# Kernel tuning notes

Measured on AMD Instinct MI355X. Metric: run time of the kernel, lower is better.

Reference implementation:

```python
import jax, jax.numpy as jnp
import numpy as np

N = 100000
E = 1600000
IN, HID, OUT = 128, 128, 64


def sage_conv(x, edge_index, W_l, W_r, b):
    # PyG SAGEConv with mean aggregation:
    # out = mean_{j in N(i)} x_j @ W_l + x_i @ W_r + b
    src, dst = edge_index[0], edge_index[1]
    msgs = x[src]                                            # [E, D] gather
    summed = jax.ops.segment_sum(msgs, dst, num_segments=N)  # [N, D] scatter-add
    deg = jax.ops.segment_sum(jnp.ones((E,), x.dtype), dst, num_segments=N)
    mean = summed / jnp.maximum(deg, 1.0)[:, None]
    return mean @ W_l + x @ W_r + b


def setup_inputs() -> dict:
    key = jax.random.key(0)
    ks = jax.random.split(key, 8)
    x = jax.random.normal(ks[0], (N, IN), dtype=jnp.float32)
    edge_index = jax.random.randint(ks[1], (2, E), 0, N, dtype=jnp.int64)
    s1 = 1.0 / np.sqrt(IN)
    s2 = 1.0 / np.sqrt(HID)
    W1_l = jax.random.uniform(ks[2], (IN, HID), jnp.float32, -s1, s1)
    W1_r = jax.random.uniform(ks[3], (IN, HID), jnp.float32, -s1, s1)
    b1 = jnp.zeros((HID,), jnp.float32)
    W2_l = jax.random.uniform(ks[4], (HID, OUT), jnp.float32, -s2, s2)
    W2_r = jax.random.uniform(ks[5], (HID, OUT), jnp.float32, -s2, s2)
    b2 = jnp.zeros((OUT,), jnp.float32)
    return {"x": x, "edge_index": edge_index, "W1_l": W1_l, "W1_r": W1_r,
            "b1": b1, "W2_l": W2_l, "W2_r": W2_r, "b2": b2}


def reference(x, edge_index, W1_l, W1_r, b1, W2_l, W2_r, b2):
    h = sage_conv(x, edge_index, W1_l, W1_r, b1)
    h = jax.nn.relu(h)
    out = sage_conv(h, edge_index, W2_l, W2_r, b2)
    return out
```

## Files before the change

kernel.cpp:

```cpp
#include <hip/hip_runtime.h>

#define NN 100000
#define NE 1600000
#define KB 782
#define BSH 7
#define MAXB 4096
#define PBLK 400

#define OFF_CC    0
#define OFF_RST   1024
#define OFF_RDG   101120
#define OFF_STAGE 201216
#define OFF_XB    3404288
#define OFF_XF8   9810432
#define OFF_MEANB 13013504
#define OFF_W1LP  25825792
#define OFF_W1RP  (25825792 + 8192)
#define OFF_W2LP  (25825792 + 16384)
#define OFF_W2RP  (25825792 + 20480)

typedef __bf16 bf16x8 __attribute__((ext_vector_type(8)));
typedef float f32x4 __attribute__((ext_vector_type(4)));
typedef float f32x2 __attribute__((ext_vector_type(2)));

static __device__ __forceinline__ ushort f2bf(float f) {
    unsigned u = __float_as_uint(f);
    return (ushort)((u + 0x7fffu + ((u >> 16) & 1u)) >> 16);
}
static __device__ __forceinline__ float bflo(unsigned u) { return __uint_as_float(u << 16); }
static __device__ __forceinline__ float bfhi(unsigned u) { return __uint_as_float(u & 0xffff0000u); }

__global__ __launch_bounds__(1024) void cpart_kernel(const int* __restrict__ src,
                                                     const int* __restrict__ dst,
                                                     int* __restrict__ cc,
                                                     unsigned* __restrict__ stage) {
    __shared__ int hist[KB];
    __shared__ int cur[KB];
    int t = threadIdx.x;
    int e0 = blockIdx.x * (NE / PBLK);
    int e1 = e0 + (NE / PBLK);
    for (int i = t; i < KB; i += 1024) hist[i] = 0;
    __syncthreads();
    for (int e = e0 + t; e < e1; e += 1024)
        atomicAdd(&hist[dst[e] >> BSH], 1);
    __syncthreads();
    for (int i = t; i < KB; i += 1024) {
        int c = hist[i];
        cur[i] = c ? atomicAdd(&cc[i], c) : 0;
    }
    __syncthreads();
    for (int e = e0 + t; e < e1; e += 1024) {
        int d = dst[e];
        int bkt = d >> BSH;
        int p = atomicAdd(&cur[bkt], 1);
        if (p < MAXB)
            stage[bkt * MAXB + p] = ((unsigned)(d & 127) << 17) | (unsigned)src[e];
    }
}

#define F2_SORT  KB
#define F2_PACKB 6
#define F2_CVT   3125
#define F2_GRID  (F2_SORT + F2_PACKB + F2_CVT)

__global__ __launch_bounds__(1024) void fused2_kernel(
    unsigned* __restrict__ stage, const int* __restrict__ cc,
    int* __restrict__ rstart, int* __restrict__ rdeg,
    const float* __restrict__ x, ushort* __restrict__ xb, unsigned* __restrict__ xf8,
    const float* __restrict__ W1l, const float* __restrict__ W1r,
    const float* __restrict__ W2l, const float* __restrict__ W2r,
    ushort* __restrict__ w1lp, ushort* __restrict__ w1rp,
    ushort* __restrict__ w2lp, ushort* __restrict__ w2rp) {
    __shared__ unsigned ssrc[MAXB];
    __shared__ int sc[128];
    __shared__ int loff[129];
    __shared__ int lcur[128];
    int bid = blockIdx.x;
    int t = threadIdx.x;

    if (bid >= F2_SORT + F2_PACKB) {
        int i = (bid - F2_SORT - F2_PACKB) * 1024 + t;
        float4 v = ((const float4*)x)[i];
        uint2 o;
        o.x = (unsigned)f2bf(v.x) | ((unsigned)f2bf(v.y) << 16);
        o.y = (unsigned)f2bf(v.z) | ((unsigned)f2bf(v.w) << 16);
        ((uint2*)xb)[i] = o;
        int p8 = __builtin_amdgcn_cvt_pk_fp8_f32(v.x, v.y, 0, false);
        p8 = __builtin_amdgcn_cvt_pk_fp8_f32(v.z, v.w, p8, true);
        xf8[i] = (unsigned)p8;
        return;
    }

    if (bid >= F2_SORT) {
        int vb = (bid - F2_SORT) * 4 + (t >> 8);
        int vt = t & 255;
        const float* W;
        ushort* out;
        int N, frag0;
        if (vb < 8)       { W = W1l; out = w1lp; N = 128; frag0 = vb * 4; }
        else if (vb < 16) { W = W1r; out = w1rp; N = 128; frag0 = (vb - 8) * 4; }
        else if (vb < 20) { W = W2l; out = w2lp; N = 64;  frag0 = (vb - 16) * 4; }
        else              { W = W2r; out = w2rp; N = 64;  frag0 = (vb - 20) * 4; }
        int lane = vt & 63;
        int frag = frag0 + (vt >> 6);
        int NT = N >> 4;
        int ktile = frag / NT, ntile = frag - ktile * NT;
        int k = ktile * 32 + (lane >> 4) * 8;
        int n = ntile * 16 + (lane & 15);
        ushort tmp[8];
#pragma unroll
        for (int j = 0; j < 8; ++j) tmp[j] = f2bf(W[(k + j) * N + n]);
        uint4 o;
        o.x = (unsigned)tmp[0] | ((unsigned)tmp[1] << 16);
        o.y = (unsigned)tmp[2] | ((unsigned)tmp[3] << 16);
        o.z = (unsigned)tmp[4] | ((unsigned)tmp[5] << 16);
        o.w = (unsigned)tmp[6] | ((unsigned)tmp[7] << 16);
        *(uint4*)&out[(frag * 64 + lane) * 8] = o;
        return;
    }

    int b = bid;
    unsigned* st = stage + b * MAXB;
    int cnt = min(cc[b], MAXB);

    if (t < 128) lcur[t] = 0;
    __syncthreads();
    for (int i = t; i < cnt; i += 1024) atomicAdd(&lcur[st[i] >> 17], 1);
    __syncthreads();
    if (t < 128) sc[t] = lcur[t];
    __syncthreads();
    for (int off = 1; off < 128; off <<= 1) {
        int v = (t < 128 && t >= off) ? sc[t - off] : 0;
        __syncthreads();
        if (t < 128) sc[t] += v;
        __syncthreads();
    }
    if (t < 128) {
        int excl = (t == 0) ? 0 : sc[t - 1];
        loff[t] = excl;
        lcur[t] = excl;
    }
    if (t == 127) loff[128] = sc[127];
    __syncthreads();
    for (int i = t; i < cnt; i += 1024) {
        unsigned v = st[i];
        int p = atomicAdd(&lcur[v >> 17], 1);
        ssrc[p] = v & 0x1FFFFu;
    }
    __syncthreads();
    for (int i = t; i < cnt; i += 1024) st[i] = ssrc[i];
    int node0 = b << BSH;
    if (t < 128 && node0 + t < NN) {
        rstart[node0 + t] = b * MAXB + loff[t];
        rdeg[node0 + t] = loff[t + 1] - loff[t];
    }
}

static __device__ __forceinline__ void accum8(float* a, uint2 u) {
    f32x2 p0 = __builtin_amdgcn_cvt_pk_f32_fp8(u.x, false);
    f32x2 p1 = __builtin_amdgcn_cvt_pk_f32_fp8(u.x, true);
    f32x2 p2 = __builtin_amdgcn_cvt_pk_f32_fp8(u.y, false);
    f32x2 p3 = __builtin_amdgcn_cvt_pk_f32_fp8(u.y, true);
    a[0] += p0.x; a[1] += p0.y; a[2] += p1.x; a[3] += p1.y;
    a[4] += p2.x; a[5] += p2.y; a[6] += p3.x; a[7] += p3.y;
}

static __device__ __forceinline__ void writeRow8(ushort* __restrict__ meanb, int node,
                                                 int l4, const float* a, int deg) {
    float inv = 1.0f / fmaxf((float)deg, 1.0f);
    uint4 o;
    o.x = (unsigned)f2bf(a[0] * inv) | ((unsigned)f2bf(a[1] * inv) << 16);
    o.y = (unsigned)f2bf(a[2] * inv) | ((unsigned)f2bf(a[3] * inv) << 16);
    o.z = (unsigned)f2bf(a[4] * inv) | ((unsigned)f2bf(a[5] * inv) << 16);
    o.w = (unsigned)f2bf(a[6] * inv) | ((unsigned)f2bf(a[7] * inv) << 16);
    *(uint4*)&meanb[node * 128 + 8 * l4] = o;
}

__global__ __launch_bounds__(256) void agg1g_kernel(const unsigned* __restrict__ es,
                                                    const int* __restrict__ rstart,
                                                    const int* __restrict__ rdeg,
                                                    const unsigned* __restrict__ xf8,
                                                    ushort* __restrict__ meanb) {
    __shared__ unsigned eidx[MAXB];
    int t = threadIdx.x;
    int node0 = blockIdx.x * 32;
    int eBase = rstart[node0];
    int last = node0 + 31;
    int cnt = rstart[last] + rdeg[last] - eBase;
    for (int i = t; i < cnt; i += 256)
        eidx[i] = __builtin_nontemporal_load(&es[eBase + i]);
    __syncthreads();

    int l4 = t & 15;
    int nA = node0 + (t >> 4) * 2;
    int nB = nA + 1;
    int sA = rstart[nA] - eBase, dA = rdeg[nA];
    int sB = rstart[nB] - eBase, dB = rdeg[nB];
    const uint2* xv = (const uint2*)xf8;
    float aA[8] = {0.f, 0.f, 0.f, 0.f, 0.f, 0.f, 0.f, 0.f};
    float aB[8] = {0.f, 0.f, 0.f, 0.f, 0.f, 0.f, 0.f, 0.f};
    int eA = 0, eB = 0;
    while (eA + 4 <= dA && eB + 4 <= dB) {
        int qa0 = eidx[sA + eA + 0], qa1 = eidx[sA + eA + 1];
        int qa2 = eidx[sA + eA + 2], qa3 = eidx[sA + eA + 3];
        int qb0 = eidx[sB + eB + 0], qb1 = eidx[sB + eB + 1];
        int qb2 = eidx[sB + eB + 2], qb3 = eidx[sB + eB + 3];
        uint2 ua0 = xv[qa0 * 16 + l4], ua1 = xv[qa1 * 16 + l4];
        uint2 ua2 = xv[qa2 * 16 + l4], ua3 = xv[qa3 * 16 + l4];
        uint2 ub0 = xv[qb0 * 16 + l4], ub1 = xv[qb1 * 16 + l4];
        uint2 ub2 = xv[qb2 * 16 + l4], ub3 = xv[qb3 * 16 + l4];
        accum8(aA, ua0); accum8(aA, ua1); accum8(aA, ua2); accum8(aA, ua3);
        accum8(aB, ub0); accum8(aB, ub1); accum8(aB, ub2); accum8(aB, ub3);
        eA += 4; eB += 4;
    }
    for (; eA + 4 <= dA; eA += 4) {
        int q0 = eidx[sA + eA + 0], q1 = eidx[sA + eA + 1];
        int q2 = eidx[sA + eA + 2], q3 = eidx[sA + eA + 3];
        uint2 u0 = xv[q0 * 16 + l4], u1 = xv[q1 * 16 + l4];
        uint2 u2 = xv[q2 * 16 + l4], u3 = xv[q3 * 16 + l4];
        accum8(aA, u0); accum8(aA, u1); accum8(aA, u2); accum8(aA, u3);
    }
    for (; eA < dA; ++eA) accum8(aA, xv[eidx[sA + eA] * 16 + l4]);
    for (; eB + 4 <= dB; eB += 4) {
        int q0 = eidx[sB + eB + 0], q1 = eidx[sB + eB + 1];
        int q2 = eidx[sB + eB + 2], q3 = eidx[sB + eB + 3];
        uint2 u0 = xv[q0 * 16 + l4], u1 = xv[q1 * 16 + l4];
        uint2 u2 = xv[q2 * 16 + l4], u3 = xv[q3 * 16 + l4];
        accum8(aB, u0); accum8(aB, u1); accum8(aB, u2); accum8(aB, u3);
    }
    for (; eB < dB; ++eB) accum8(aB, xv[eidx[sB + eB] * 16 + l4]);

    writeRow8(meanb, nA, l4, aA, dA);
    writeRow8(meanb, nB, l4, aB, dB);
}

__global__ __launch_bounds__(256) void agg2g_kernel(const unsigned* __restrict__ es,
                                                    const int* __restrict__ rstart,
                                                    const int* __restrict__ rdeg,
                                                    const ushort* __restrict__ pb,
                                                    float* __restrict__ out) {
    __shared__ unsigned eidx[MAXB];
    int t = threadIdx.x;
    int node0 = blockIdx.x * 16;
    int eBase = rstart[node0];
    int last = node0 + 15;
    int cnt = rstart[last] + rdeg[last] - eBase;
    for (int i = t; i < cnt; i += 256)
        eidx[i] = __builtin_nontemporal_load(&es[eBase + i]);
    __syncthreads();

    int l5 = t & 31;
    int nA = node0 + (t >> 5) * 2;
    int nB = nA + 1;
    int sA = rstart[nA] - eBase, dA = rdeg[nA];
    int sB = rstart[nB] - eBase, dB = rdeg[nB];
    float2 pA = *(const float2*)&out[(size_t)nA * 64 + 2 * l5];
    float2 pB = *(const float2*)&out[(size_t)nB * 64 + 2 * l5];
    const unsigned* pbu = (const unsigned*)pb;
    float a0 = 0.f, a1 = 0.f, b0 = 0.f, b1 = 0.f;
    int eA = 0, eB = 0;
    while (eA + 4 <= dA && eB + 4 <= dB) {
        int qa0 = eidx[sA + eA + 0], qa1 = eidx[sA + eA + 1];
        int qa2 = eidx[sA + eA + 2], qa3 = eidx[sA + eA + 3];
        int qb0 = eidx[sB + eB + 0], qb1 = eidx[sB + eB + 1];
        int qb2 = eidx[sB + eB + 2], qb3 = eidx[sB + eB + 3];
        unsigned ua0 = pbu[qa0 * 32 + l5], ua1 = pbu[qa1 * 32 + l5];
        unsigned ua2 = pbu[qa2 * 32 + l5], ua3 = pbu[qa3 * 32 + l5];
        unsigned ub0 = pbu[qb0 * 32 + l5], ub1 = pbu[qb1 * 32 + l5];
        unsigned ub2 = pbu[qb2 * 32 + l5], ub3 = pbu[qb3 * 32 + l5];
        a0 += bflo(ua0) + bflo(ua1) + bflo(ua2) + bflo(ua3);
        a1 += bfhi(ua0) + bfhi(ua1) + bfhi(ua2) + bfhi(ua3);
        b0 += bflo(ub0) + bflo(ub1) + bflo(ub2) + bflo(ub3);
        b1 += bfhi(ub0) + bfhi(ub1) + bfhi(ub2) + bfhi(ub3);
        eA += 4; eB += 4;
    }
    for (; eA + 4 <= dA; eA += 4) {
        int q0 = eidx[sA + eA + 0], q1 = eidx[sA + eA + 1];
        int q2 = eidx[sA + eA + 2], q3 = eidx[sA + eA + 3];
        unsigned u0 = pbu[q0 * 32 + l5], u1 = pbu[q1 * 32 + l5];
        unsigned u2 = pbu[q2 * 32 + l5], u3 = pbu[q3 * 32 + l5];
        a0 += bflo(u0) + bflo(u1) + bflo(u2) + bflo(u3);
        a1 += bfhi(u0) + bfhi(u1) + bfhi(u2) + bfhi(u3);
    }
    for (; eA < dA; ++eA) {
        unsigned u = pbu[eidx[sA + eA] * 32 + l5];
        a0 += bflo(u); a1 += bfhi(u);
    }
    for (; eB + 4 <= dB; eB += 4) {
        int q0 = eidx[sB + eB + 0], q1 = eidx[sB + eB + 1];
        int q2 = eidx[sB + eB + 2], q3 = eidx[sB + eB + 3];
        unsigned u0 = pbu[q0 * 32 + l5], u1 = pbu[q1 * 32 + l5];
        unsigned u2 = pbu[q2 * 32 + l5], u3 = pbu[q3 * 32 + l5];
        b0 += bflo(u0) + bflo(u1) + bflo(u2) + bflo(u3);
        b1 += bfhi(u0) + bfhi(u1) + bfhi(u2) + bfhi(u3);
    }
    for (; eB < dB; ++eB) {
        unsigned u = pbu[eidx[sB + eB] * 32 + l5];
        b0 += bflo(u); b1 += bfhi(u);
    }
    float invA = 1.0f / fmaxf((float)dA, 1.0f);
    float invB = 1.0f / fmaxf((float)dB, 1.0f);
    float2 oA = {pA.x + a0 * invA, pA.y + a1 * invA};
    float2 oB = {pB.x + b0 * invB, pB.y + b1 * invB};
    *(float2*)&out[(size_t)nA * 64 + 2 * l5] = oA;
    *(float2*)&out[(size_t)nB * 64 + 2 * l5] = oB;
}

__global__ __launch_bounds__(256) void gemm1_kernel(const ushort* __restrict__ meanb,
                                                    const ushort* __restrict__ xb,
                                                    const ushort* __restrict__ w1lp,
                                                    const ushort* __restrict__ w1rp,
                                                    const float* __restrict__ b1,
                                                    const ushort* __restrict__ w2lp,
                                                    const ushort* __restrict__ w2rp,
                                                    const float* __restrict__ b2,
                                                    ushort* __restrict__ pb,
                                                    float* __restrict__ out) {
    __shared__ ushort As[64 * 136];
    __shared__ ushort Ws[16384];
    int t = threadIdx.x;
    int node0 = blockIdx.x * 64;
    int w = t >> 6, l = t & 63;
    int lrow = w * 16 + (l & 15);
    int lkq = (l >> 4) * 8;
    int cq = l & 15, rq = (l >> 4) * 4;

    f32x4 acc[8];
#pragma unroll
    for (int i = 0; i < 8; ++i) acc[i] = (f32x4){0.f, 0.f, 0.f, 0.f};

    {
        const uint4* g = (const uint4*)(meanb + (size_t)node0 * 128);
#pragma unroll
        for (int i = 0; i < 4; ++i) {
            int chunk = t + 256 * i;
            *(uint4*)&As[(chunk >> 4) * 136 + (chunk & 15) * 8] = g[chunk];
        }
        const uint4* wsrc = (const uint4*)w1lp;
#pragma unroll
        for (int i = 0; i < 8; ++i)
            ((uint4*)Ws)[t + 256 * i] = wsrc[t + 256 * i];
    }
    __syncthreads();
#pragma unroll
    for (int kt = 0; kt < 4; ++kt) {
        bf16x8 a = *(const bf16x8*)&As[lrow * 136 + kt * 32 + lkq];
        const bf16x8* bp = (const bf16x8*)Ws + (kt * 8) * 64 + l;
#pragma unroll
        for (int nt = 0; nt < 8; ++nt)
            acc[nt] = __builtin_amdgcn_mfma_f32_16x16x32_bf16(a, bp[nt * 64], acc[nt], 0, 0, 0);
    }
    __syncthreads();

    {
        const uint4* g = (const uint4*)(xb + (size_t)node0 * 128);
#pragma unroll
        for (int i = 0; i < 4; ++i) {
            int chunk = t + 256 * i;
            *(uint4*)&As[(chunk >> 4) * 136 + (chunk & 15) * 8] = g[chunk];
        }
        const uint4* wsrc = (const uint4*)w1rp;
#pragma unroll
        for (int i = 0; i < 8; ++i)
            ((uint4*)Ws)[t + 256 * i] = wsrc[t + 256 * i];
    }
    __syncthreads();
#pragma unroll
    for (int kt = 0; kt < 4; ++kt) {
        bf16x8 a = *(const bf16x8*)&As[lrow * 136 + kt * 32 + lkq];
        const bf16x8* bp = (const bf16x8*)Ws + (kt * 8) * 64 + l;
#pragma unroll
        for (int nt = 0; nt < 8; ++nt)
            acc[nt] = __builtin_amdgcn_mfma_f32_16x16x32_bf16(a, bp[nt * 64], acc[nt], 0, 0, 0);
    }
    __syncthreads();

#pragma unroll
    for (int nt = 0; nt < 8; ++nt) {
        int n = nt * 16 + cq;
        float bias = b1[n];
#pragma unroll
        for (int r = 0; r < 4; ++r) {
            float hv = fmaxf(acc[nt][r] + bias, 0.0f);
            As[(w * 16 + rq + r) * 136 + n] = f2bf(hv);
        }
    }
    {
        const uint4* wl = (const uint4*)w2lp;
        const uint4* wr = (const uint4*)w2rp;
#pragma unroll
        for (int i = 0; i < 4; ++i) {
            int chunk = t + 256 * i;
            ((uint4*)Ws)[chunk] = wl[chunk];
            ((uint4*)Ws)[1024 + chunk] = wr[chunk];
        }
    }
    __syncthreads();

    f32x4 acc2[4];
    f32x4 acc3[4];
#pragma unroll
    for (int i = 0; i < 4; ++i) {
        acc2[i] = (f32x4){0.f, 0.f, 0.f, 0.f};
        acc3[i] = (f32x4){0.f, 0.f, 0.f, 0.f};
    }
#pragma unroll
    for (int kt = 0; kt < 4; ++kt) {
        bf16x8 a = *(const bf16x8*)&As[lrow * 136 + kt * 32 + lkq];
        const bf16x8* bpl = (const bf16x8*)Ws + (kt * 4) * 64 + l;
        const bf16x8* bpr = (const bf16x8*)(Ws + 8192) + (kt * 4) * 64 + l;
#pragma unroll
        for (int nt = 0; nt < 4; ++nt) {
            acc2[nt] = __builtin_amdgcn_mfma_f32_16x16x32_bf16(a, bpl[nt * 64], acc2[nt], 0, 0, 0);
            acc3[nt] = __builtin_amdgcn_mfma_f32_16x16x32_bf16(a, bpr[nt * 64], acc3[nt], 0, 0, 0);
        }
    }

#pragma unroll
    for (int nt = 0; nt < 4; ++nt) {
        int n = nt * 16 + cq;
        float bias = b2[n];
#pragma unroll
        for (int r = 0; r < 4; ++r) {
            int row = node0 + w * 16 + rq + r;
            if (row < NN)
                out[(size_t)row * 64 + n] = acc3[nt][r] + bias;
        }
    }

    __syncthreads();
#pragma unroll
    for (int nt = 0; nt < 4; ++nt)
#pragma unroll
        for (int r = 0; r < 4; ++r)
            As[(w * 16 + rq + r) * 136 + nt * 16 + cq] = f2bf(acc2[nt][r]);
    __syncthreads();
    {
        uint4* g = (uint4*)(pb + (size_t)node0 * 64);
#pragma unroll
        for (int i = 0; i < 2; ++i) {
            int chunk = t + 256 * i;
            if (node0 + (chunk >> 3) < NN)
                g[chunk] = *(const uint4*)&As[(chunk >> 3) * 136 + (chunk & 7) * 8];
        }
    }
}

extern "C" void kernel_launch(void* const* d_in, const int* in_sizes, int n_in,
                              void* d_out, int out_size, void* d_ws, size_t ws_size,
                              hipStream_t stream) {
    const float* x   = (const float*)d_in[0];
    const int*   ei  = (const int*)d_in[1];
    const float* W1l = (const float*)d_in[2];
    const float* W1r = (const float*)d_in[3];
    const float* b1  = (const float*)d_in[4];
    const float* W2l = (const float*)d_in[5];
    const float* W2r = (const float*)d_in[6];
    const float* b2  = (const float*)d_in[7];

    const int* src = ei;
    const int* dst = ei + NE;

    int*      ws_i   = (int*)d_ws;
    int*      cc     = ws_i + OFF_CC;
    int*      rstart = ws_i + OFF_RST;
    int*      rdeg   = ws_i + OFF_RDG;
    unsigned* stage  = (unsigned*)(ws_i + OFF_STAGE);
    ushort*   xb     = (ushort*)(ws_i + OFF_XB);
    unsigned* xf8    = (unsigned*)(ws_i + OFF_XF8);
    ushort*   pb     = (ushort*)(ws_i + OFF_XF8);
    ushort*   meanb  = (ushort*)(ws_i + OFF_MEANB);
    ushort*   w1lp   = (ushort*)(ws_i + OFF_W1LP);
    ushort*   w1rp   = (ushort*)(ws_i + OFF_W1RP);
    ushort*   w2lp   = (ushort*)(ws_i + OFF_W2LP);
    ushort*   w2rp   = (ushort*)(ws_i + OFF_W2RP);

    (void)hipMemsetAsync(cc, 0, 1024 * sizeof(int), stream);

    cpart_kernel<<<PBLK, 1024, 0, stream>>>(src, dst, cc, stage);
    fused2_kernel<<<F2_GRID, 1024, 0, stream>>>(
        stage, cc, rstart, rdeg, x, xb, xf8,
        W1l, W1r, W2l, W2r, w1lp, w1rp, w2lp, w2rp);

    agg1g_kernel<<<NN / 32, 256, 0, stream>>>(stage, rstart, rdeg, xf8, meanb);
    gemm1_kernel<<<(NN + 63) / 64, 256, 0, stream>>>(meanb, xb, w1lp, w1rp, b1,
                                                     w2lp, w2rp, b2, pb, (float*)d_out);

    agg2g_kernel<<<NN / 16, 256, 0, stream>>>(stage, rstart, rdeg, pb, (float*)d_out);
}
```

Baseline: 236.6 us.

## Fuse layer-1 mean aggregation into the GEMM kernel via shared memory

Merges the layer-1 neighbor aggregation kernel with the dense GEMM kernel. Each 64-node block gathers its edge lists into the shared weight buffer, aggregates fp8 features directly into the shared A tile, then runs both layer-1 matmuls and the layer-2 projections. This removes one launch and the round trip of the bf16 mean matrix through global memory. In exchange, each block holds more shared memory and has less parallelism during the gather phase. The rstart/rdeg bounds guard is dropped so padded nodes get entries, and pb moves to a separate buffer.

```diff
diff --git a/kernel.cpp b/kernel.cpp
--- a/kernel.cpp
+++ b/kernel.cpp
@@ -150,11 +150,13 @@
     __syncthreads();
     for (int i = t; i < cnt; i += 1024) st[i] = ssrc[i];
     int node0 = b << BSH;
-    if (t < 128 && node0 + t < NN) {
+    if (t < 128) {
         rstart[node0 + t] = b * MAXB + loff[t];
         rdeg[node0 + t] = loff[t + 1] - loff[t];
     }
 }
+
+#define L1_GRID 1563
 
 static __device__ __forceinline__ void accum8(float* a, uint2 u) {
     f32x2 p0 = __builtin_amdgcn_cvt_pk_f32_fp8(u.x, false);
@@ -165,73 +167,182 @@
     a[4] += p2.x; a[5] += p2.y; a[6] += p3.x; a[7] += p3.y;
 }
 
-static __device__ __forceinline__ void writeRow8(ushort* __restrict__ meanb, int node,
-                                                 int l4, const float* a, int deg) {
-    float inv = 1.0f / fmaxf((float)deg, 1.0f);
-    uint4 o;
-    o.x = (unsigned)f2bf(a[0] * inv) | ((unsigned)f2bf(a[1] * inv) << 16);
-    o.y = (unsigned)f2bf(a[2] * inv) | ((unsigned)f2bf(a[3] * inv) << 16);
-    o.z = (unsigned)f2bf(a[4] * inv) | ((unsigned)f2bf(a[5] * inv) << 16);
-    o.w = (unsigned)f2bf(a[6] * inv) | ((unsigned)f2bf(a[7] * inv) << 16);
-    *(uint4*)&meanb[node * 128 + 8 * l4] = o;
-}
-
-__global__ __launch_bounds__(256) void agg1g_kernel(const unsigned* __restrict__ es,
-                                                    const int* __restrict__ rstart,
-                                                    const int* __restrict__ rdeg,
-                                                    const unsigned* __restrict__ xf8,
-                                                    ushort* __restrict__ meanb) {
-    __shared__ unsigned eidx[MAXB];
+__global__ __launch_bounds__(256) void l1_kernel(const unsigned* __restrict__ es,
+                                                 const int* __restrict__ rstart,
+                                                 const int* __restrict__ rdeg,
+                                                 const unsigned* __restrict__ xf8,
+                                                 const ushort* __restrict__ xb,
+                                                 const ushort* __restrict__ w1lp,
+                                                 const ushort* __restrict__ w1rp,
+                                                 const float* __restrict__ b1,
+                                                 const ushort* __restrict__ w2lp,
+                                                 const ushort* __restrict__ w2rp,
+                                                 const float* __restrict__ b2,
+                                                 ushort* __restrict__ pb,
+                                                 float* __restrict__ out) {
+    __shared__ ushort As[64 * 136];
+    __shared__ ushort WsBuf[16384];
+    unsigned* eidx = (unsigned*)WsBuf;
+
     int t = threadIdx.x;
-    int node0 = blockIdx.x * 32;
+    int node0 = blockIdx.x * 64;
+
     int eBase = rstart[node0];
-    int last = node0 + 31;
-    int cnt = rstart[last] + rdeg[last] - eBase;
+    int lastN = node0 + 63;
+    int cnt = rstart[lastN] + rdeg[lastN] - eBase;
     for (int i = t; i < cnt; i += 256)
         eidx[i] = __builtin_nontemporal_load(&es[eBase + i]);
     __syncthreads();
 
-    int l4 = t & 15;
-    int nA = node0 + (t >> 4) * 2;
-    int nB = nA + 1;
-    int sA = rstart[nA] - eBase, dA = rdeg[nA];
-    int sB = rstart[nB] - eBase, dB = rdeg[nB];
-    const uint2* xv = (const uint2*)xf8;
-    float aA[8] = {0.f, 0.f, 0.f, 0.f, 0.f, 0.f, 0.f, 0.f};
-    float aB[8] = {0.f, 0.f, 0.f, 0.f, 0.f, 0.f, 0.f, 0.f};
-    int eA = 0, eB = 0;
-    while (eA + 4 <= dA && eB + 4 <= dB) {
-        int qa0 = eidx[sA + eA + 0], qa1 = eidx[sA + eA + 1];
-        int qa2 = eidx[sA + eA + 2], qa3 = eidx[sA + eA + 3];
-        int qb0 = eidx[sB + eB + 0], qb1 = eidx[sB + eB + 1];
-        int qb2 = eidx[sB + eB + 2], qb3 = eidx[sB + eB + 3];
-        uint2 ua0 = xv[qa0 * 16 + l4], ua1 = xv[qa1 * 16 + l4];
-        uint2 ua2 = xv[qa2 * 16 + l4], ua3 = xv[qa3 * 16 + l4];
-        uint2 ub0 = xv[qb0 * 16 + l4], ub1 = xv[qb1 * 16 + l4];
-        uint2 ub2 = xv[qb2 * 16 + l4], ub3 = xv[qb3 * 16 + l4];
-        accum8(aA, ua0); accum8(aA, ua1); accum8(aA, ua2); accum8(aA, ua3);
-        accum8(aB, ub0); accum8(aB, ub1); accum8(aB, ub2); accum8(aB, ub3);
-        eA += 4; eB += 4;
-    }
-    for (; eA + 4 <= dA; eA += 4) {
-        int q0 = eidx[sA + eA + 0], q1 = eidx[sA + eA + 1];
-        int q2 = eidx[sA + eA + 2], q3 = eidx[sA + eA + 3];
-        uint2 u0 = xv[q0 * 16 + l4], u1 = xv[q1 * 16 + l4];
-        uint2 u2 = xv[q2 * 16 + l4], u3 = xv[q3 * 16 + l4];
-        accum8(aA, u0); accum8(aA, u1); accum8(aA, u2); accum8(aA, u3);
-    }
-    for (; eA < dA; ++eA) accum8(aA, xv[eidx[sA + eA] * 16 + l4]);
-    for (; eB + 4 <= dB; eB += 4) {
-        int q0 = eidx[sB + eB + 0], q1 = eidx[sB + eB + 1];
-        int q2 = eidx[sB + eB + 2], q3 = eidx[sB + eB + 3];
-        uint2 u0 = xv[q0 * 16 + l4], u1 = xv[q1 * 16 + l4];
-        uint2 u2 = xv[q2 * 16 + l4], u3 = xv[q3 * 16 + l4];
-        accum8(aB, u0); accum8(aB, u1); accum8(aB, u2); accum8(aB, u3);
-    }
-    for (; eB < dB; ++eB) accum8(aB, xv[eidx[sB + eB] * 16 + l4]);
-
-    writeRow8(meanb, nA, l4, aA, dA);
-    writeRow8(meanb, nB, l4, aB, dB);
+    {
+        int l4 = t & 15;
+        int g = t >> 4;
+        const uint2* xv = (const uint2*)xf8;
+#pragma unroll
+        for (int k = 0; k < 4; ++k) {
+            int nl = g * 4 + k;
+            int node = node0 + nl;
+            int s0 = rstart[node] - eBase;
+            int deg = rdeg[node];
+            float a[8] = {0.f, 0.f, 0.f, 0.f, 0.f, 0.f, 0.f, 0.f};
+            int e = 0;
+            for (; e + 4 <= deg; e += 4) {
+                int q0 = eidx[s0 + e + 0], q1 = eidx[s0 + e + 1];
+                int q2 = eidx[s0 + e + 2], q3 = eidx[s0 + e + 3];
+                uint2 u0 = xv[q0 * 16 + l4], u1 = xv[q1 * 16 + l4];
+                uint2 u2 = xv[q2 * 16 + l4], u3 = xv[q3 * 16 + l4];
+                accum8(a, u0); accum8(a, u1); accum8(a, u2); accum8(a, u3);
+            }
+            for (; e < deg; ++e) accum8(a, xv[eidx[s0 + e] * 16 + l4]);
+            float inv = 1.0f / fmaxf((float)deg, 1.0f);
+            uint4 o;
+            o.x = (unsigned)f2bf(a[0] * inv) | ((unsigned)f2bf(a[1] * inv) << 16);
+            o.y = (unsigned)f2bf(a[2] * inv) | ((unsigned)f2bf(a[3] * inv) << 16);
+            o.z = (unsigned)f2bf(a[4] * inv) | ((unsigned)f2bf(a[5] * inv) << 16);
+            o.w = (unsigned)f2bf(a[6] * inv) | ((unsigned)f2bf(a[7] * inv) << 16);
+            *(uint4*)&As[nl * 136 + 8 * l4] = o;
+        }
+    }
+    __syncthreads();
+
+    int w = t >> 6, l = t & 63;
+    int lrow = w * 16 + (l & 15);
+    int lkq = (l >> 4) * 8;
+    int cq = l & 15, rq = (l >> 4) * 4;
+
+    f32x4 acc[8];
+#pragma unroll
+    for (int i = 0; i < 8; ++i) acc[i] = (f32x4){0.f, 0.f, 0.f, 0.f};
+
+    {
+        const uint4* wsrc = (const uint4*)w1lp;
+#pragma unroll
+        for (int i = 0; i < 8; ++i)
+            ((uint4*)WsBuf)[t + 256 * i] = wsrc[t + 256 * i];
+    }
+    __syncthreads();
+#pragma unroll
+    for (int kt = 0; kt < 4; ++kt) {
+        bf16x8 a = *(const bf16x8*)&As[lrow * 136 + kt * 32 + lkq];
+        const bf16x8* bp = (const bf16x8*)WsBuf + (kt * 8) * 64 + l;
+#pragma unroll
+        for (int nt = 0; nt < 8; ++nt)
+            acc[nt] = __builtin_amdgcn_mfma_f32_16x16x32_bf16(a, bp[nt * 64], acc[nt], 0, 0, 0);
+    }
+    __syncthreads();
+
+    {
+        const uint4* g2 = (const uint4*)(xb + (size_t)node0 * 128);
+#pragma unroll
+        for (int i = 0; i < 4; ++i) {
+            int chunk = t + 256 * i;
+            *(uint4*)&As[(chunk >> 4) * 136 + (chunk & 15) * 8] = g2[chunk];
+        }
+        const uint4* wsrc = (const uint4*)w1rp;
+#pragma unroll
+        for (int i = 0; i < 8; ++i)
+            ((uint4*)WsBuf)[t + 256 * i] = wsrc[t + 256 * i];
+    }
+    __syncthreads();
+#pragma unroll
+    for (int kt = 0; kt < 4; ++kt) {
+        bf16x8 a = *(const bf16x8*)&As[lrow * 136 + kt * 32 + lkq];
+        const bf16x8* bp = (const bf16x8*)WsBuf + (kt * 8) * 64 + l;
+#pragma unroll
+        for (int nt = 0; nt < 8; ++nt)
+            acc[nt] = __builtin_amdgcn_mfma_f32_16x16x32_bf16(a, bp[nt * 64], acc[nt], 0, 0, 0);
+    }
+    __syncthreads();
+
+#pragma unroll
+    for (int nt = 0; nt < 8; ++nt) {
+        int n = nt * 16 + cq;
+        float bias = b1[n];
+#pragma unroll
+        for (int r = 0; r < 4; ++r) {
+            float hv = fmaxf(acc[nt][r] + bias, 0.0f);
+            As[(w * 16 + rq + r) * 136 + n] = f2bf(hv);
+        }
+    }
+    {
+        const uint4* wl = (const uint4*)w2lp;
+        const uint4* wr = (const uint4*)w2rp;
+#pragma unroll
+        for (int i = 0; i < 4; ++i) {
+            int chunk = t + 256 * i;
+            ((uint4*)WsBuf)[chunk] = wl[chunk];
+            ((uint4*)WsBuf)[1024 + chunk] = wr[chunk];
+        }
+    }
+    __syncthreads();
+
+    f32x4 acc2[4];
+    f32x4 acc3[4];
+#pragma unroll
+    for (int i = 0; i < 4; ++i) {
+        acc2[i] = (f32x4){0.f, 0.f, 0.f, 0.f};
+        acc3[i] = (f32x4){0.f, 0.f, 0.f, 0.f};
+    }
+#pragma unroll
+    for (int kt = 0; kt < 4; ++kt) {
+        bf16x8 a = *(const bf16x8*)&As[lrow * 136 + kt * 32 + lkq];
+        const bf16x8* bpl = (const bf16x8*)WsBuf + (kt * 4) * 64 + l;
+        const bf16x8* bpr = (const bf16x8*)(WsBuf + 8192) + (kt * 4) * 64 + l;
+#pragma unroll
+        for (int nt = 0; nt < 4; ++nt) {
+            acc2[nt] = __builtin_amdgcn_mfma_f32_16x16x32_bf16(a, bpl[nt * 64], acc2[nt], 0, 0, 0);
+            acc3[nt] = __builtin_amdgcn_mfma_f32_16x16x32_bf16(a, bpr[nt * 64], acc3[nt], 0, 0, 0);
+        }
+    }
+
+#pragma unroll
+    for (int nt = 0; nt < 4; ++nt) {
+        int n = nt * 16 + cq;
+        float bias = b2[n];
+#pragma unroll
+        for (int r = 0; r < 4; ++r) {
+            int row = node0 + w * 16 + rq + r;
+            if (row < NN)
+                out[(size_t)row * 64 + n] = acc3[nt][r] + bias;
+        }
+    }
+
+    __syncthreads();
+#pragma unroll
+    for (int nt = 0; nt < 4; ++nt)
+#pragma unroll
+        for (int r = 0; r < 4; ++r)
+            As[(w * 16 + rq + r) * 136 + nt * 16 + cq] = f2bf(acc2[nt][r]);
+    __syncthreads();
+    {
+        uint4* g2 = (uint4*)(pb + (size_t)node0 * 64);
+#pragma unroll
+        for (int i = 0; i < 2; ++i) {
+            int chunk = t + 256 * i;
+            if (node0 + (chunk >> 3) < NN)
+                g2[chunk] = *(const uint4*)&As[(chunk >> 3) * 136 + (chunk & 7) * 8];
+        }
+    }
 }
 
 __global__ __launch_bounds__(256) void agg2g_kernel(const unsigned* __restrict__ es,
@@ -306,146 +417,6 @@
     *(float2*)&out[(size_t)nB * 64 + 2 * l5] = oB;
 }
 
-__global__ __launch_bounds__(256) void gemm1_kernel(const ushort* __restrict__ meanb,
-                                                    const ushort* __restrict__ xb,
-                                                    const ushort* __restrict__ w1lp,
-                                                    const ushort* __restrict__ w1rp,
-                                                    const float* __restrict__ b1,
-                                                    const ushort* __restrict__ w2lp,
-                                                    const ushort* __restrict__ w2rp,
-                                                    const float* __restrict__ b2,
-                                                    ushort* __restrict__ pb,
-                                                    float* __restrict__ out) {
-    __shared__ ushort As[64 * 136];
-    __shared__ ushort Ws[16384];
-    int t = threadIdx.x;
-    int node0 = blockIdx.x * 64;
-    int w = t >> 6, l = t & 63;
-    int lrow = w * 16 + (l & 15);
-    int lkq = (l >> 4) * 8;
-    int cq = l & 15, rq = (l >> 4) * 4;
-
-    f32x4 acc[8];
-#pragma unroll
-    for (int i = 0; i < 8; ++i) acc[i] = (f32x4){0.f, 0.f, 0.f, 0.f};
-
-    {
-        const uint4* g = (const uint4*)(meanb + (size_t)node0 * 128);
-#pragma unroll
-        for (int i = 0; i < 4; ++i) {
-            int chunk = t + 256 * i;
-            *(uint4*)&As[(chunk >> 4) * 136 + (chunk & 15) * 8] = g[chunk];
-        }
-        const uint4* wsrc = (const uint4*)w1lp;
-#pragma unroll
-        for (int i = 0; i < 8; ++i)
-            ((uint4*)Ws)[t + 256 * i] = wsrc[t + 256 * i];
-    }
-    __syncthreads();
-#pragma unroll
-    for (int kt = 0; kt < 4; ++kt) {
-        bf16x8 a = *(const bf16x8*)&As[lrow * 136 + kt * 32 + lkq];
-        const bf16x8* bp = (const bf16x8*)Ws + (kt * 8) * 64 + l;
-#pragma unroll
-        for (int nt = 0; nt < 8; ++nt)
-            acc[nt] = __builtin_amdgcn_mfma_f32_16x16x32_bf16(a, bp[nt * 64], acc[nt], 0, 0, 0);
-    }
-    __syncthreads();
-
-    {
-        const uint4* g = (const uint4*)(xb + (size_t)node0 * 128);
-#pragma unroll
-        for (int i = 0; i < 4; ++i) {
-            int chunk = t + 256 * i;
-            *(uint4*)&As[(chunk >> 4) * 136 + (chunk & 15) * 8] = g[chunk];
-        }
-        const uint4* wsrc = (const uint4*)w1rp;
-#pragma unroll
-        for (int i = 0; i < 8; ++i)
-            ((uint4*)Ws)[t + 256 * i] = wsrc[t + 256 * i];
-    }
-    __syncthreads();
-#pragma unroll
-    for (int kt = 0; kt < 4; ++kt) {
-        bf16x8 a = *(const bf16x8*)&As[lrow * 136 + kt * 32 + lkq];
-        const bf16x8* bp = (const bf16x8*)Ws + (kt * 8) * 64 + l;
-#pragma unroll
-        for (int nt = 0; nt < 8; ++nt)
-            acc[nt] = __builtin_amdgcn_mfma_f32_16x16x32_bf16(a, bp[nt * 64], acc[nt], 0, 0, 0);
-    }
-    __syncthreads();
-
-#pragma unroll
-    for (int nt = 0; nt < 8; ++nt) {
-        int n = nt * 16 + cq;
-        float bias = b1[n];
-#pragma unroll
-        for (int r = 0; r < 4; ++r) {
-            float hv = fmaxf(acc[nt][r] + bias, 0.0f);
-            As[(w * 16 + rq + r) * 136 + n] = f2bf(hv);
-        }
-    }
-    {
-        const uint4* wl = (const uint4*)w2lp;
-        const uint4* wr = (const uint4*)w2rp;
-#pragma unroll
-        for (int i = 0; i < 4; ++i) {
-            int chunk = t + 256 * i;
-            ((uint4*)Ws)[chunk] = wl[chunk];
-            ((uint4*)Ws)[1024 + chunk] = wr[chunk];
-        }
-    }
-    __syncthreads();
-
-    f32x4 acc2[4];
-    f32x4 acc3[4];
-#pragma unroll
-    for (int i = 0; i < 4; ++i) {
-        acc2[i] = (f32x4){0.f, 0.f, 0.f, 0.f};
-        acc3[i] = (f32x4){0.f, 0.f, 0.f, 0.f};
-    }
-#pragma unroll
-    for (int kt = 0; kt < 4; ++kt) {
-        bf16x8 a = *(const bf16x8*)&As[lrow * 136 + kt * 32 + lkq];
-        const bf16x8* bpl = (const bf16x8*)Ws + (kt * 4) * 64 + l;
-        const bf16x8* bpr = (const bf16x8*)(Ws + 8192) + (kt * 4) * 64 + l;
-#pragma unroll
-        for (int nt = 0; nt < 4; ++nt) {
-            acc2[nt] = __builtin_amdgcn_mfma_f32_16x16x32_bf16(a, bpl[nt * 64], acc2[nt], 0, 0, 0);
-            acc3[nt] = __builtin_amdgcn_mfma_f32_16x16x32_bf16(a, bpr[nt * 64], acc3[nt], 0, 0, 0);
-        }
-    }
-
-#pragma unroll
-    for (int nt = 0; nt < 4; ++nt) {
-        int n = nt * 16 + cq;
-        float bias = b2[n];
-#pragma unroll
-        for (int r = 0; r < 4; ++r) {
-            int row = node0 + w * 16 + rq + r;
-            if (row < NN)
-                out[(size_t)row * 64 + n] = acc3[nt][r] + bias;
-        }
-    }
-
-    __syncthreads();
-#pragma unroll
-    for (int nt = 0; nt < 4; ++nt)
-#pragma unroll
-        for (int r = 0; r < 4; ++r)
-            As[(w * 16 + rq + r) * 136 + nt * 16 + cq] = f2bf(acc2[nt][r]);
-    __syncthreads();
-    {
-        uint4* g = (uint4*)(pb + (size_t)node0 * 64);
-#pragma unroll
-        for (int i = 0; i < 2; ++i) {
-            int chunk = t + 256 * i;
-            if (node0 + (chunk >> 3) < NN)
-                g[chunk] = *(const uint4*)&As[(chunk >> 3) * 136 + (chunk & 7) * 8];
-        }
-    }
-}
-
 extern "C" void kernel_launch(void* const* d_in, const int* in_sizes, int n_in,
                               void* d_out, int out_size, void* d_ws, size_t ws_size,
                               hipStream_t stream) {
@@ -468,8 +439,7 @@
     unsigned* stage  = (unsigned*)(ws_i + OFF_STAGE);
     ushort*   xb     = (ushort*)(ws_i + OFF_XB);
     unsigned* xf8    = (unsigned*)(ws_i + OFF_XF8);
-    ushort*   pb     = (ushort*)(ws_i + OFF_XF8);
-    ushort*   meanb  = (ushort*)(ws_i + OFF_MEANB);
+    ushort*   pb     = (ushort*)(ws_i + OFF_MEANB);
     ushort*   w1lp   = (ushort*)(ws_i + OFF_W1LP);
     ushort*   w1rp   = (ushort*)(ws_i + OFF_W1RP);
     ushort*   w2lp   = (ushort*)(ws_i + OFF_W2LP);
@@ -482,9 +452,9 @@
         stage, cc, rstart, rdeg, x, xb, xf8,
         W1l, W1r, W2l, W2r, w1lp, w1rp, w2lp, w2rp);
 
-    agg1g_kernel<<<NN / 32, 256, 0, stream>>>(stage, rstart, rdeg, xf8, meanb);
-    gemm1_kernel<<<(NN + 63) / 64, 256, 0, stream>>>(meanb, xb, w1lp, w1rp, b1,
-                                                     w2lp, w2rp, b2, pb, (float*)d_out);
+    l1_kernel<<<L1_GRID, 256, 0, stream>>>(stage, rstart, rdeg, xf8, xb,
+                                           w1lp, w1rp, b1, w2lp, w2rp, b2,
+                                           pb, (float*)d_out);
 
     agg2g_kernel<<<NN / 16, 256, 0, stream>>>(stage, rstart, rdeg, pb, (float*)d_out);
 }
```

New measurement: 244.3 us. +3.2%, slower.
